# Kernel tuning notes

Measured on AMD Instinct MI355X. Metric: run time of the kernel, lower is better.

The kernel has to match this reference:

```python
import jax, jax.numpy as jnp
import numpy as np

GROUPS = 1024
K_N = 32
FEAT_DIM = 64
EPS = 1e-05


def farthest_point_sample(xyz, npoint):
    # xyz: [B, N, 3] -> centroids [B, npoint] int32
    # Original torch code starts from a random point; we use index 0 for determinism.
    B, N, _ = xyz.shape

    def step(carry, _):
        distance, farthest = carry
        centroid = jnp.take_along_axis(xyz, farthest[:, None, None], axis=1)  # [B,1,3]
        dist = jnp.sum((xyz - centroid) ** 2, axis=-1)  # [B,N]
        distance = jnp.minimum(distance, dist)
        new_far = jnp.argmax(distance, axis=-1).astype(jnp.int32)
        return (distance, new_far), farthest

    init = (jnp.full((B, N), 1e10, dtype=xyz.dtype), jnp.zeros((B,), jnp.int32))
    _, cents = jax.lax.scan(step, init, None, length=npoint)
    return cents.T  # [B, npoint]


def index_points(points, idx):
    # points: [B, N, C]; idx: [B, ...] -> [B, ..., C]
    B = points.shape[0]
    bidx = jnp.arange(B).reshape((B,) + (1,) * (idx.ndim - 1))
    return points[bidx, idx]


def square_distance(src, dst):
    # src [B,S,C], dst [B,N,C] -> [B,S,N]
    d = -2.0 * jnp.einsum('bsc,bnc->bsn', src, dst)
    d = d + jnp.sum(src ** 2, -1)[:, :, None]
    d = d + jnp.sum(dst ** 2, -1)[:, None, :]
    return d


def setup_inputs() -> dict:
    key = jax.random.key(0)
    k1, k2 = jax.random.split(key)
    xyz = jax.random.normal(k1, (8, 3, 4096), dtype=jnp.float32)
    feats = jax.random.normal(k2, (8, FEAT_DIM, 4096), dtype=jnp.float32)
    affine_alpha_p = jnp.ones((1, 1, 1, FEAT_DIM), jnp.float32)
    affine_beta_p = jnp.zeros((1, 1, 1, FEAT_DIM), jnp.float32)
    return {"xyz": xyz, "feats": feats,
            "affine_alpha_p": affine_alpha_p, "affine_beta_p": affine_beta_p}


def reference(xyz, feats, affine_alpha_p, affine_beta_p):
    xyz = jnp.transpose(xyz, (0, 2, 1))      # [B,N,3]
    feats = jnp.transpose(feats, (0, 2, 1))  # [B,N,D]
    B, N, _ = xyz.shape
    S, k = GROUPS, K_N

    fps_idx = farthest_point_sample(xyz, S)          # [B,S]
    new_xyz = index_points(xyz, fps_idx)             # [B,S,3]
    new_feats = index_points(feats, fps_idx)         # [B,S,D]

    sqr = square_distance(new_xyz, xyz)              # [B,S,N]
    _, idx = jax.lax.top_k(-sqr, k)                  # smallest-k -> [B,S,k]
    grouped = index_points(feats, idx)               # [B,S,k,D]

    mean = new_feats[:, :, None, :]                  # [B,S,1,D]
    diff = grouped - mean
    # torch.std over flattened per-batch, unbiased (ddof=1)
    std = jnp.std(diff.reshape(B, -1), axis=-1, ddof=1)[:, None, None, None]
    grouped = diff / (std + EPS)
    grouped = affine_alpha_p * grouped + affine_beta_p

    point_feats = jnp.concatenate(
        [grouped, grouped - new_feats[:, :, None, :]], axis=-1)  # [B,S,k,2D]

    new_feats_out = jnp.transpose(new_feats, (0, 2, 1))          # [B,D,S]
    new_xyz_out = jnp.transpose(new_xyz, (0, 2, 1))              # [B,3,S]
    point_feats_out = jnp.transpose(point_feats, (0, 3, 1, 2))   # [B,2D,S,k]
    return (new_xyz_out, new_feats_out, point_feats_out)
```

## Files before the change

kernel.cpp:

```cpp
#include <hip/hip_runtime.h>

#define NPTS 4096
#define NSAMP 1024
#define KNN_K 32
#define FDIM 64
#define EPSF 1e-5f

typedef float v2f __attribute__((ext_vector_type(2)));

#define DPP_MAX64(CTRL)                                                          \
  {                                                                              \
    unsigned _olo = (unsigned)__builtin_amdgcn_update_dpp(0, (int)klo, CTRL,     \
                                                          0xf, 0xf, true);       \
    unsigned _ohi = (unsigned)__builtin_amdgcn_update_dpp(0, (int)khi, CTRL,     \
                                                          0xf, 0xf, true);       \
    unsigned long long _ok = ((unsigned long long)_ohi << 32) | _olo;            \
    unsigned long long _ck = ((unsigned long long)khi << 32) | klo;              \
    if (_ok > _ck) { klo = _olo; khi = _ohi; }                                   \
  }

__device__ __forceinline__ unsigned long long umax64(unsigned long long a,
                                                     unsigned long long b) {
  return a > b ? a : b;
}

__global__ __launch_bounds__(256) void fps_kernel(const float* __restrict__ xyz,
                                                  int* __restrict__ fps_idx,
                                                  float* __restrict__ sqnorm) {
#pragma clang fp contract(off)
  __shared__ float4 pts[NPTS];
  __shared__ unsigned long long skeys[2][4];
  __shared__ int fpsb[NSAMP];
  const int b = blockIdx.x, t = threadIdx.x;
  const int lane = t & 63, w = t >> 6;
  const float* xb = xyz + (size_t)b * 3 * NPTS;
  v2f px[8], py[8], pz[8];
  unsigned long long key[16];
  unsigned rik[16];
  const unsigned initb = __float_as_uint(1e10f);
#pragma unroll
  for (int j = 0; j < 8; ++j) {
    int p0 = (2 * j) * 256 + t, p1 = (2 * j + 1) * 256 + t;
    float x0 = xb[p0], y0 = xb[NPTS + p0], z0 = xb[2 * NPTS + p0];
    float x1 = xb[p1], y1 = xb[NPTS + p1], z1 = xb[2 * NPTS + p1];
    float sq0 = __fadd_rn(__fadd_rn(__fmul_rn(x0, x0), __fmul_rn(y0, y0)),
                          __fmul_rn(z0, z0));
    float sq1 = __fadd_rn(__fadd_rn(__fmul_rn(x1, x1), __fmul_rn(y1, y1)),
                          __fmul_rn(z1, z1));
    pts[p0] = make_float4(x0, y0, z0, sq0);
    pts[p1] = make_float4(x1, y1, z1, sq1);
    sqnorm[b * NPTS + p0] = sq0;
    sqnorm[b * NPTS + p1] = sq1;
    px[j].x = x0; px[j].y = x1;
    py[j].x = y0; py[j].y = y1;
    pz[j].x = z0; pz[j].y = z1;
    rik[2 * j] = 4095u - (unsigned)p0;
    rik[2 * j + 1] = 4095u - (unsigned)p1;
    key[2 * j] = ((unsigned long long)initb << 12) | rik[2 * j];
    key[2 * j + 1] = ((unsigned long long)initb << 12) | rik[2 * j + 1];
  }
  if (t == 0) fpsb[0] = 0;
  __syncthreads();
  float4 c = pts[0];
  for (int it = 1; it < NSAMP; ++it) {
    v2f vcx, vcy, vcz;
    vcx.x = c.x; vcx.y = c.x;
    vcy.x = c.y; vcy.y = c.y;
    vcz.x = c.z; vcz.y = c.z;
#pragma unroll
    for (int j = 0; j < 8; ++j) {
      v2f dx = px[j] - vcx;
      v2f dy = py[j] - vcy;
      v2f dz = pz[j] - vcz;
      v2f dd = (dx * dx + dy * dy) + dz * dz;
      unsigned long long k0 =
          ((unsigned long long)__float_as_uint(dd.x) << 12) | rik[2 * j];
      unsigned long long k1 =
          ((unsigned long long)__float_as_uint(dd.y) << 12) | rik[2 * j + 1];
      if (k0 < key[2 * j]) key[2 * j] = k0;
      if (k1 < key[2 * j + 1]) key[2 * j + 1] = k1;
    }
    unsigned long long a0 = umax64(key[0], key[1]),   a1 = umax64(key[2], key[3]);
    unsigned long long a2 = umax64(key[4], key[5]),   a3 = umax64(key[6], key[7]);
    unsigned long long a4 = umax64(key[8], key[9]),   a5 = umax64(key[10], key[11]);
    unsigned long long a6 = umax64(key[12], key[13]), a7 = umax64(key[14], key[15]);
    unsigned long long b0 = umax64(a0, a1), b1 = umax64(a2, a3);
    unsigned long long b2 = umax64(a4, a5), b3 = umax64(a6, a7);
    unsigned long long m = umax64(umax64(b0, b1), umax64(b2, b3));
    unsigned klo = (unsigned)m, khi = (unsigned)(m >> 32);
    DPP_MAX64(0x111)
    DPP_MAX64(0x112)
    DPP_MAX64(0x114)
    DPP_MAX64(0x118)
    DPP_MAX64(0x142)
    DPP_MAX64(0x143)
    if (lane == 63) skeys[it & 1][w] = ((unsigned long long)khi << 32) | klo;
    __syncthreads();
    unsigned long long kk2 = skeys[it & 1][lane & 3];
    klo = (unsigned)kk2;
    khi = (unsigned)(kk2 >> 32);
    DPP_MAX64(0x111)
    DPP_MAX64(0x112)
    unsigned flo = (unsigned)__builtin_amdgcn_readlane((int)klo, 3);
    int far = 4095 - (int)(flo & 0xfffu);
    if (t == 0) fpsb[it] = far;
    c = pts[far];
  }
  __syncthreads();
#pragma unroll
  for (int k = 0; k < 4; ++k)
    fps_idx[b * NSAMP + k * 256 + t] = fpsb[k * 256 + t];
}

__global__ __launch_bounds__(256) void gather_feats_kernel(const float* __restrict__ feats,
                                                           const int* __restrict__ fps,
                                                           float* __restrict__ out1,
                                                           float* __restrict__ nf) {
  int i = blockIdx.x * 256 + threadIdx.x;
  int s = i & 1023, c = (i >> 10) & 63, b = i >> 16;
  int p = fps[(b << 10) + s];
  float v = feats[((size_t)(b * 64 + c)) * NPTS + p];
  out1[(b * 64 + c) * 1024 + s] = v;
  nf[(((b << 10) + s) << 6) + c] = v;
}

__global__ __launch_bounds__(256) void gather_xyz_kernel(const float* __restrict__ xyz,
                                                         const float* __restrict__ sqnorm,
                                                         const int* __restrict__ fps,
                                                         float* __restrict__ out0,
                                                         float4* __restrict__ nx4) {
  int i = blockIdx.x * 256 + threadIdx.x;
  int b = i >> 10, s = i & 1023;
  int p = fps[i];
  const float* xb = xyz + (size_t)b * 3 * NPTS;
  float x = xb[p], y = xb[NPTS + p], z = xb[2 * NPTS + p];
  nx4[i] = make_float4(x, y, z, sqnorm[b * NPTS + p]);
  out0[(b * 3 + 0) * 1024 + s] = x;
  out0[(b * 3 + 1) * 1024 + s] = y;
  out0[(b * 3 + 2) * 1024 + s] = z;
}

__device__ __forceinline__ unsigned long long mk_key(float xn, float yn, float zn,
                                                     float sq, float cx, float cy,
                                                     float cz, float src2, int n) {
  float dot = __fmaf_rn(zn, cz, __fmaf_rn(yn, cy, __fmul_rn(xn, cx)));
  float d = __fadd_rn(__fadd_rn(__fmul_rn(-2.0f, dot), src2), sq);
  unsigned mb = __float_as_uint(d);
  mb = (mb & 0x80000000u) ? ~mb : (mb | 0x80000000u);
  return ((unsigned long long)mb << 32) | (unsigned)n;
}

__global__ __launch_bounds__(256, 2) void knn_kernel(const float* __restrict__ xyz,
                                                     const float* __restrict__ sqnorm,
                                                     const float4* __restrict__ nx4,
                                                     int* __restrict__ knn) {
  const int lane = threadIdx.x & 63;
  const int w = threadIdx.x >> 6;
  const int row = blockIdx.x * 4 + w;
  const int b = row >> 10;
  const float4 c4 = nx4[row];
  const float cx = c4.x, cy = c4.y, cz = c4.z, src2 = c4.w;
  const float4* x4 = (const float4*)(xyz + (size_t)b * 3 * NPTS);
  const float4* y4 = (const float4*)(xyz + (size_t)b * 3 * NPTS + NPTS);
  const float4* z4 = (const float4*)(xyz + (size_t)b * 3 * NPTS + 2 * NPTS);
  const float4* s4 = (const float4*)(sqnorm + (size_t)b * NPTS);
  unsigned long long key[64];
#pragma unroll
  for (int jj = 0; jj < 16; ++jj) {
    int vi = jj * 64 + lane;
    float4 xv = x4[vi], yv = y4[vi], zv = z4[vi], sv = s4[vi];
    int n0 = vi * 4;
    key[jj * 4 + 0] = mk_key(xv.x, yv.x, zv.x, sv.x, cx, cy, cz, src2, n0);
    key[jj * 4 + 1] = mk_key(xv.y, yv.y, zv.y, sv.y, cx, cy, cz, src2, n0 + 1);
    key[jj * 4 + 2] = mk_key(xv.z, yv.z, zv.z, sv.z, cx, cy, cz, src2, n0 + 2);
    key[jj * 4 + 3] = mk_key(xv.w, yv.w, zv.w, sv.w, cx, cy, cz, src2, n0 + 3);
  }
  unsigned long long last = 0ull;
  const int out_base = row * KNN_K;
#pragma unroll 1
  for (int r = 0; r < KNN_K; ++r) {
    unsigned long long cur = ~0ull;
#pragma unroll
    for (int j = 0; j < 64; ++j) {
      unsigned long long k = key[j];
      if (k > last && k < cur) cur = k;
    }
#pragma unroll
    for (int off = 32; off > 0; off >>= 1) {
      unsigned long long o = __shfl_xor(cur, off);
      cur = (o < cur) ? o : cur;
    }
    last = cur;
    if (lane == r) knn[out_base + r] = (int)(unsigned)(cur & 0xffffffffull);
  }
}

__global__ __launch_bounds__(256) void stats_kernel(const float* __restrict__ feats,
                                                    const float* __restrict__ nf,
                                                    const int* __restrict__ knn,
                                                    double* __restrict__ stats) {
  const int b = blockIdx.x >> 5;
  const int chunk = blockIdx.x & 31;
  const int base = chunk * 65536;
  double sm = 0.0, sq = 0.0;
  for (int i = 0; i < 256; ++i) {
    int e = base + i * 256 + threadIdx.x;
    int c = e >> 15;
    int sk = e & 32767;
    int s = sk >> 5, j = sk & 31;
    int p = knn[((((b << 10) + s)) << 5) + j];
    float f = feats[((size_t)(b * 64 + c)) * NPTS + p];
    float m = nf[(((b << 10) + s) << 6) + c];
    double d = (double)__fsub_rn(f, m);
    sm += d;
    sq += d * d;
  }
#pragma unroll
  for (int off = 32; off > 0; off >>= 1) {
    sm += __shfl_down(sm, off);
    sq += __shfl_down(sq, off);
  }
  __shared__ double red[8];
  int w = threadIdx.x >> 6;
  if ((threadIdx.x & 63) == 0) { red[w * 2] = sm; red[w * 2 + 1] = sq; }
  __syncthreads();
  if (threadIdx.x == 0) {
    atomicAdd(&stats[b * 2 + 0], red[0] + red[2] + red[4] + red[6]);
    atomicAdd(&stats[b * 2 + 1], red[1] + red[3] + red[5] + red[7]);
  }
}

__global__ __launch_bounds__(256) void out_kernel(const float* __restrict__ feats,
                                                  const float* __restrict__ nf,
                                                  const int* __restrict__ knn,
                                                  const double* __restrict__ stats,
                                                  const float* __restrict__ alpha,
                                                  const float* __restrict__ beta,
                                                  float* __restrict__ out2) {
  const int plane = blockIdx.x;
  const int b = plane >> 6, c = plane & 63;
  const int sk = blockIdx.y * 256 + threadIdx.x;
  const int s = sk >> 5, j = sk & 31;
  const double n = 2097152.0;
  double sm = stats[b * 2], sqs = stats[b * 2 + 1];
  double var = (sqs - sm * sm / n) / (n - 1.0);
  float stdf = (float)sqrt(var);
  float denom = stdf + EPSF;
  int p = knn[((((b << 10) + s)) << 5) + j];
  float f = feats[((size_t)(b * 64 + c)) * NPTS + p];
  float m = nf[(((b << 10) + s) << 6) + c];
  float diff = __fsub_rn(f, m);
  float g = alpha[c] * (diff / denom) + beta[c];
  size_t o1 = (((size_t)(b * 128 + c) << 10) + (size_t)s) * 32 + j;
  size_t o2 = (((size_t)(b * 128 + 64 + c) << 10) + (size_t)s) * 32 + j;
  out2[o1] = g;
  out2[o2] = g - m;
}

extern "C" void kernel_launch(void* const* d_in, const int* in_sizes, int n_in,
                              void* d_out, int out_size, void* d_ws, size_t ws_size,
                              hipStream_t stream) {
  (void)in_sizes; (void)n_in; (void)out_size; (void)ws_size;
  const float* xyz   = (const float*)d_in[0];
  const float* feats = (const float*)d_in[1];
  const float* alpha = (const float*)d_in[2];
  const float* beta  = (const float*)d_in[3];
  float* out  = (float*)d_out;
  float* out0 = out;
  float* out1 = out + 24576;
  float* out2 = out + 24576 + 524288;

  char* ws = (char*)d_ws;
  int*    fps   = (int*)ws;
  float*  sqn   = (float*)(ws + 32768);
  float4* nx4   = (float4*)(ws + 163840);
  float*  nf    = (float*)(ws + 294912);
  int*    knn   = (int*)(ws + 2392064);
  double* stats = (double*)(ws + 3440640);

  hipMemsetAsync(stats, 0, 128, stream);
  fps_kernel<<<8, 256, 0, stream>>>(xyz, fps, sqn);
  gather_feats_kernel<<<2048, 256, 0, stream>>>(feats, fps, out1, nf);
  gather_xyz_kernel<<<32, 256, 0, stream>>>(xyz, sqn, fps, out0, nx4);
  knn_kernel<<<2048, 256, 0, stream>>>(xyz, sqn, nx4, knn);
  stats_kernel<<<256, 256, 0, stream>>>(feats, nf, knn, stats);
  out_kernel<<<dim3(512, 128), 256, 0, stream>>>(feats, nf, knn, stats, alpha, beta, out2);
}
```

Before: 1.106 ms.

## Restructure FPS: 512 threads, float min/max, carry centroid coords through reduction

Result: slower. 1.247 ms (+12.8%).

```diff
diff --git a/kernel.cpp b/kernel.cpp
--- a/kernel.cpp
+++ b/kernel.cpp
@@ -8,108 +8,116 @@
 
 typedef float v2f __attribute__((ext_vector_type(2)));
 
-#define DPP_MAX64(CTRL)                                                          \
-  {                                                                              \
+#define DPP_STEP(CTRL)                                                           \
+  do {                                                                           \
     unsigned _olo = (unsigned)__builtin_amdgcn_update_dpp(0, (int)klo, CTRL,     \
                                                           0xf, 0xf, true);       \
     unsigned _ohi = (unsigned)__builtin_amdgcn_update_dpp(0, (int)khi, CTRL,     \
                                                           0xf, 0xf, true);       \
+    unsigned _ox = (unsigned)__builtin_amdgcn_update_dpp(0, (int)wx, CTRL, 0xf,  \
+                                                         0xf, true);             \
+    unsigned _oy = (unsigned)__builtin_amdgcn_update_dpp(0, (int)wy, CTRL, 0xf,  \
+                                                         0xf, true);             \
+    unsigned _oz = (unsigned)__builtin_amdgcn_update_dpp(0, (int)wz, CTRL, 0xf,  \
+                                                         0xf, true);             \
     unsigned long long _ok = ((unsigned long long)_ohi << 32) | _olo;            \
     unsigned long long _ck = ((unsigned long long)khi << 32) | klo;              \
-    if (_ok > _ck) { klo = _olo; khi = _ohi; }                                   \
-  }
-
-__device__ __forceinline__ unsigned long long umax64(unsigned long long a,
-                                                     unsigned long long b) {
-  return a > b ? a : b;
-}
-
-__global__ __launch_bounds__(256) void fps_kernel(const float* __restrict__ xyz,
+    if (_ok > _ck) { klo = _olo; khi = _ohi; wx = _ox; wy = _oy; wz = _oz; }     \
+  } while (0)
+
+__global__ __launch_bounds__(512) void fps_kernel(const float* __restrict__ xyz,
                                                   int* __restrict__ fps_idx,
                                                   float* __restrict__ sqnorm) {
 #pragma clang fp contract(off)
-  __shared__ float4 pts[NPTS];
-  __shared__ unsigned long long skeys[2][4];
+  __shared__ uint4 slotA[2][8];
+  __shared__ unsigned slotZ[2][8];
   __shared__ int fpsb[NSAMP];
   const int b = blockIdx.x, t = threadIdx.x;
   const int lane = t & 63, w = t >> 6;
   const float* xb = xyz + (size_t)b * 3 * NPTS;
-  v2f px[8], py[8], pz[8];
-  unsigned long long key[16];
-  unsigned rik[16];
-  const unsigned initb = __float_as_uint(1e10f);
-#pragma unroll
-  for (int j = 0; j < 8; ++j) {
-    int p0 = (2 * j) * 256 + t, p1 = (2 * j + 1) * 256 + t;
+  v2f px[4], py[4], pz[4];
+  float dist[8];
+#pragma unroll
+  for (int j = 0; j < 4; ++j) {
+    int p0 = (2 * j) * 512 + t, p1 = (2 * j + 1) * 512 + t;
     float x0 = xb[p0], y0 = xb[NPTS + p0], z0 = xb[2 * NPTS + p0];
     float x1 = xb[p1], y1 = xb[NPTS + p1], z1 = xb[2 * NPTS + p1];
     float sq0 = __fadd_rn(__fadd_rn(__fmul_rn(x0, x0), __fmul_rn(y0, y0)),
                           __fmul_rn(z0, z0));
     float sq1 = __fadd_rn(__fadd_rn(__fmul_rn(x1, x1), __fmul_rn(y1, y1)),
                           __fmul_rn(z1, z1));
-    pts[p0] = make_float4(x0, y0, z0, sq0);
-    pts[p1] = make_float4(x1, y1, z1, sq1);
     sqnorm[b * NPTS + p0] = sq0;
     sqnorm[b * NPTS + p1] = sq1;
     px[j].x = x0; px[j].y = x1;
     py[j].x = y0; py[j].y = y1;
     pz[j].x = z0; pz[j].y = z1;
-    rik[2 * j] = 4095u - (unsigned)p0;
-    rik[2 * j + 1] = 4095u - (unsigned)p1;
-    key[2 * j] = ((unsigned long long)initb << 12) | rik[2 * j];
-    key[2 * j + 1] = ((unsigned long long)initb << 12) | rik[2 * j + 1];
+    dist[2 * j] = 1e10f;
+    dist[2 * j + 1] = 1e10f;
   }
   if (t == 0) fpsb[0] = 0;
-  __syncthreads();
-  float4 c = pts[0];
+  float cx = xb[0], cy = xb[NPTS], cz = xb[2 * NPTS];
   for (int it = 1; it < NSAMP; ++it) {
     v2f vcx, vcy, vcz;
-    vcx.x = c.x; vcx.y = c.x;
-    vcy.x = c.y; vcy.y = c.y;
-    vcz.x = c.z; vcz.y = c.z;
-#pragma unroll
-    for (int j = 0; j < 8; ++j) {
+    vcx.x = cx; vcx.y = cx;
+    vcy.x = cy; vcy.y = cy;
+    vcz.x = cz; vcz.y = cz;
+#pragma unroll
+    for (int j = 0; j < 4; ++j) {
       v2f dx = px[j] - vcx;
       v2f dy = py[j] - vcy;
       v2f dz = pz[j] - vcz;
       v2f dd = (dx * dx + dy * dy) + dz * dz;
-      unsigned long long k0 =
-          ((unsigned long long)__float_as_uint(dd.x) << 12) | rik[2 * j];
-      unsigned long long k1 =
-          ((unsigned long long)__float_as_uint(dd.y) << 12) | rik[2 * j + 1];
-      if (k0 < key[2 * j]) key[2 * j] = k0;
-      if (k1 < key[2 * j + 1]) key[2 * j + 1] = k1;
-    }
-    unsigned long long a0 = umax64(key[0], key[1]),   a1 = umax64(key[2], key[3]);
-    unsigned long long a2 = umax64(key[4], key[5]),   a3 = umax64(key[6], key[7]);
-    unsigned long long a4 = umax64(key[8], key[9]),   a5 = umax64(key[10], key[11]);
-    unsigned long long a6 = umax64(key[12], key[13]), a7 = umax64(key[14], key[15]);
-    unsigned long long b0 = umax64(a0, a1), b1 = umax64(a2, a3);
-    unsigned long long b2 = umax64(a4, a5), b3 = umax64(a6, a7);
-    unsigned long long m = umax64(umax64(b0, b1), umax64(b2, b3));
-    unsigned klo = (unsigned)m, khi = (unsigned)(m >> 32);
-    DPP_MAX64(0x111)
-    DPP_MAX64(0x112)
-    DPP_MAX64(0x114)
-    DPP_MAX64(0x118)
-    DPP_MAX64(0x142)
-    DPP_MAX64(0x143)
-    if (lane == 63) skeys[it & 1][w] = ((unsigned long long)khi << 32) | klo;
+      dist[2 * j] = fminf(dist[2 * j], dd.x);
+      dist[2 * j + 1] = fminf(dist[2 * j + 1], dd.y);
+    }
+    float m0 = fmaxf(dist[0], dist[1]), m1 = fmaxf(dist[2], dist[3]);
+    float m2 = fmaxf(dist[4], dist[5]), m3 = fmaxf(dist[6], dist[7]);
+    float mv = fmaxf(fmaxf(m0, m1), fmaxf(m2, m3));
+    unsigned ri = 7u;
+    float sx = px[3].y, sy = py[3].y, sz = pz[3].y;
+#pragma unroll
+    for (int k = 6; k >= 0; --k) {
+      bool e = (dist[k] == mv);
+      ri = e ? (unsigned)k : ri;
+      sx = e ? ((k & 1) ? px[k >> 1].y : px[k >> 1].x) : sx;
+      sy = e ? ((k & 1) ? py[k >> 1].y : py[k >> 1].x) : sy;
+      sz = e ? ((k & 1) ? pz[k >> 1].y : pz[k >> 1].x) : sz;
+    }
+    unsigned idx = (ri << 9) + (unsigned)t;
+    unsigned mvb = __float_as_uint(mv);
+    unsigned klo = (mvb << 12) | (4095u - idx);
+    unsigned khi = mvb >> 20;
+    unsigned wx = __float_as_uint(sx), wy = __float_as_uint(sy),
+             wz = __float_as_uint(sz);
+    DPP_STEP(0x111);
+    DPP_STEP(0x112);
+    DPP_STEP(0x114);
+    DPP_STEP(0x118);
+    DPP_STEP(0x142);
+    DPP_STEP(0x143);
+    const int buf = it & 1;
+    if (lane == 63) {
+      slotA[buf][w] = make_uint4(klo, khi, wx, wy);
+      slotZ[buf][w] = wz;
+    }
     __syncthreads();
-    unsigned long long kk2 = skeys[it & 1][lane & 3];
-    klo = (unsigned)kk2;
-    khi = (unsigned)(kk2 >> 32);
-    DPP_MAX64(0x111)
-    DPP_MAX64(0x112)
-    unsigned flo = (unsigned)__builtin_amdgcn_readlane((int)klo, 3);
+    uint4 q = slotA[buf][lane & 7];
+    unsigned zz = slotZ[buf][lane & 7];
+    klo = q.x; khi = q.y; wx = q.z; wy = q.w; wz = zz;
+    DPP_STEP(0x111);
+    DPP_STEP(0x112);
+    DPP_STEP(0x114);
+    unsigned flo = (unsigned)__builtin_amdgcn_readlane((int)klo, 7);
     int far = 4095 - (int)(flo & 0xfffu);
+    cx = __uint_as_float((unsigned)__builtin_amdgcn_readlane((int)wx, 7));
+    cy = __uint_as_float((unsigned)__builtin_amdgcn_readlane((int)wy, 7));
+    cz = __uint_as_float((unsigned)__builtin_amdgcn_readlane((int)wz, 7));
     if (t == 0) fpsb[it] = far;
-    c = pts[far];
   }
   __syncthreads();
 #pragma unroll
-  for (int k = 0; k < 4; ++k)
-    fps_idx[b * NSAMP + k * 256 + t] = fpsb[k * 256 + t];
+  for (int k = 0; k < 2; ++k)
+    fps_idx[b * NSAMP + k * 512 + t] = fpsb[k * 512 + t];
 }
 
 __global__ __launch_bounds__(256) void gather_feats_kernel(const float* __restrict__ feats,
@@ -279,7 +287,7 @@
   double* stats = (double*)(ws + 3440640);
 
   hipMemsetAsync(stats, 0, 128, stream);
-  fps_kernel<<<8, 256, 0, stream>>>(xyz, fps, sqn);
+  fps_kernel<<<8, 512, 0, stream>>>(xyz, fps, sqn);
   gather_feats_kernel<<<2048, 256, 0, stream>>>(feats, fps, out1, nf);
   gather_xyz_kernel<<<32, 256, 0, stream>>>(xyz, sqn, fps, out0, nx4);
   knn_kernel<<<2048, 256, 0, stream>>>(xyz, sqn, nx4, knn);
```
